# Performance work log

Hardware: AMD Instinct MI355X
Metric: run time of the kernel (lower is better)

## Reference

```python
import jax, jax.numpy as jnp
import numpy as np

N, E, IN, H, C, T = 50000, 800000, 128, 64, 64, 2
F1, FO1 = H, H // T   # conv1: per-tower in/out feats
F2, FO2 = H, C // T   # conv2
STD_EPS = 1e-5
BN_EPS = 1e-5


def setup_inputs() -> dict:
    key = jax.random.key(0)
    ks = jax.random.split(key, 12)
    rn = lambda k, s, sc=0.05: jax.random.normal(k, s, jnp.float32) * sc
    return {
        "x": jax.random.normal(ks[0], (N, IN), jnp.float32),
        "embed_W": rn(ks[1], (IN, H)),
        "embed_b": jnp.zeros((H,), jnp.float32),
        "pre_W1": rn(ks[2], (T, 2 * F1, F1)),
        "pre_b1": jnp.zeros((T, F1), jnp.float32),
        "post_W1": rn(ks[3], (T, 13 * F1, FO1)),
        "post_b1": jnp.zeros((T, FO1), jnp.float32),
        "lin_W1": rn(ks[4], (H, H)),
        "lin_b1": jnp.zeros((H,), jnp.float32),
        "bn_gamma": jnp.ones((H,), jnp.float32),
        "bn_beta": jnp.zeros((H,), jnp.float32),
        "pre_W2": rn(ks[5], (T, 2 * F2, F2)),
        "pre_b2": jnp.zeros((T, F2), jnp.float32),
        "post_W2": rn(ks[6], (T, 13 * F2, FO2)),
        "post_b2": jnp.zeros((T, FO2), jnp.float32),
        "lin_W2": rn(ks[7], (C, C)),
        "lin_b2": jnp.zeros((C,), jnp.float32),
        "src": jax.random.randint(ks[8], (E,), 0, N, jnp.int32),
        "dst": jax.random.randint(ks[9], (E,), 0, N, jnp.int32),
    }


def _pna_conv(h, src, dst, deg_raw, degc, avg_log, preW, preb, postW, postb, linW, linb):
    # h: [N, F] node feats; messages flow src -> dst, aggregated at dst.
    m = jnp.concatenate([h[dst], h[src]], axis=-1)            # [E, 2F]  (cat[x_i, x_j])
    m = jnp.einsum('ef,tfg->etg', m, preW) + preb[None]       # [E, T, F] per-tower pre-NN
    seg = lambda v: jax.ops.segment_sum(v, dst, num_segments=N)
    cnt = degc[:, None, None]                                 # clamped degree >= 1
    has = (deg_raw > 0)[:, None, None]
    mean = seg(m) / cnt                                       # [N, T, F]
    mean_sq = seg(m * m) / cnt
    mn = jnp.where(has, jax.ops.segment_min(m, dst, num_segments=N), 0.0)
    mx = jnp.where(has, jax.ops.segment_max(m, dst, num_segments=N), 0.0)
    std = jnp.sqrt(jax.nn.relu(mean_sq - mean * mean) + STD_EPS)
    agg = jnp.concatenate([mean, mn, mx, std], axis=-1)       # [N, T, 4F]
    ld = jnp.log(degc + 1.0)[:, None, None]
    out = jnp.concatenate([agg, agg * (ld / avg_log), agg * (avg_log / ld)], axis=-1)  # [N, T, 12F]
    F = h.shape[-1]
    out = jnp.concatenate([jnp.broadcast_to(h[:, None, :], (N, T, F)), out], axis=-1)  # [N, T, 13F]
    out = jnp.einsum('ntf,tfg->ntg', out, postW) + postb[None]  # [N, T, FO] per-tower post-NN
    return out.reshape(N, -1) @ linW + linb                    # final mixing Linear(out, out)


def reference(x, embed_W, embed_b, pre_W1, pre_b1, post_W1, post_b1, lin_W1, lin_b1,
              bn_gamma, bn_beta, pre_W2, pre_b2, post_W2, post_b2, lin_W2, lin_b2,
              src, dst):
    deg_raw = jax.ops.segment_sum(jnp.ones((E,), jnp.float32), dst, num_segments=N)
    degc = jnp.maximum(deg_raw, 1.0)
    avg_log = jnp.mean(jnp.log(deg_raw + 1.0))  # avg_deg['log'] from the graph's degrees
    h = x @ embed_W + embed_b
    h = _pna_conv(h, src, dst, deg_raw, degc, avg_log,
                  pre_W1, pre_b1, post_W1, post_b1, lin_W1, lin_b1)
    mu = jnp.mean(h, axis=0)
    var = jnp.mean((h - mu) ** 2, axis=0)
    h = bn_gamma * (h - mu) / jnp.sqrt(var + BN_EPS) + bn_beta
    h = jax.nn.relu(h)  # dropout is identity in eval mode
    return _pna_conv(h, src, dst, deg_raw, degc, avg_log,
                     pre_W2, pre_b2, post_W2, post_b2, lin_W2, lin_b2)
```

## Files before the change

kernel.cpp:

```cpp
#include <hip/hip_runtime.h>

#define N_NODES 50000
#define E_EDGES 800000
#define IN_F    128
#define H_F     64
#define STD_EPS 1e-5f
#define BN_EPS  1e-5f

__global__ __launch_bounds__(256) void k_hist(const int* __restrict__ dst,
                                              int* __restrict__ deg) {
  int e = blockIdx.x * 256 + threadIdx.x;
  if (e < E_EDGES) atomicAdd(&deg[dst[e]], 1);
}

__global__ __launch_bounds__(256) void k_scan_part(const int* __restrict__ deg,
                                                   int* __restrict__ partials,
                                                   float* __restrict__ scalars) {
  __shared__ int red[256];
  __shared__ float redf[256];
  int base = blockIdx.x * 1024;
  int s = 0; float ls = 0.f;
  for (int j = threadIdx.x; j < 1024; j += 256) {
    int i = base + j;
    if (i < N_NODES) { int d = deg[i]; s += d; ls += logf((float)d + 1.0f); }
  }
  red[threadIdx.x] = s; redf[threadIdx.x] = ls; __syncthreads();
  for (int st = 128; st > 0; st >>= 1) {
    if (threadIdx.x < st) {
      red[threadIdx.x] += red[threadIdx.x + st];
      redf[threadIdx.x] += redf[threadIdx.x + st];
    }
    __syncthreads();
  }
  if (threadIdx.x == 0) {
    partials[blockIdx.x] = red[0];
    atomicAdd(&scalars[0], redf[0]);
  }
}

__global__ void k_scan_mid(int* __restrict__ partials, int nblk,
                           float* __restrict__ scalars) {
  if (threadIdx.x == 0) {
    int run = 0;
    for (int b = 0; b < nblk; b++) { int v = partials[b]; partials[b] = run; run += v; }
    scalars[1] = scalars[0] / (float)N_NODES;
  }
}

__global__ __launch_bounds__(256) void k_scan_final(const int* __restrict__ deg,
                                                    const int* __restrict__ partials,
                                                    int* __restrict__ row_ptr,
                                                    int* __restrict__ cursor) {
  __shared__ int ts[256];
  int base = blockIdx.x * 1024 + threadIdx.x * 4;
  int d[4]; int s = 0;
#pragma unroll
  for (int j = 0; j < 4; j++) {
    int i = base + j;
    d[j] = (i < N_NODES) ? deg[i] : 0;
    s += d[j];
  }
  ts[threadIdx.x] = s; __syncthreads();
  for (int off = 1; off < 256; off <<= 1) {
    int t = (threadIdx.x >= off) ? ts[threadIdx.x - off] : 0;
    __syncthreads();
    ts[threadIdx.x] += t;
    __syncthreads();
  }
  int excl = (threadIdx.x > 0) ? ts[threadIdx.x - 1] : 0;
  int run = partials[blockIdx.x] + excl;
#pragma unroll
  for (int j = 0; j < 4; j++) {
    int i = base + j;
    if (i < N_NODES) { row_ptr[i] = run; cursor[i] = run; run += d[j]; }
  }
  if (blockIdx.x == 0 && threadIdx.x == 0) row_ptr[N_NODES] = E_EDGES;
}

__global__ __launch_bounds__(256) void k_scatter(const int* __restrict__ src,
                                                 const int* __restrict__ dst,
                                                 int* __restrict__ cursor,
                                                 int* __restrict__ csr_src) {
  int e = blockIdx.x * 256 + threadIdx.x;
  if (e < E_EDGES) {
    int d = dst[e];
    int p = atomicAdd(&cursor[d], 1);
    csr_src[p] = src[e];
  }
}

__global__ __launch_bounds__(256) void k_transpose(const float* __restrict__ pW1,
                                                   const float* __restrict__ pW2,
                                                   const float* __restrict__ lW1,
                                                   const float* __restrict__ lW2,
                                                   float* __restrict__ pWT,
                                                   float* __restrict__ lWT) {
  int idx = blockIdx.x * 256 + threadIdx.x;
  if (idx < 106496) {
    int layer = idx / 53248, r = idx % 53248;
    int t = r / 26624, r2 = r % 26624;
    int fb = r2 / 128, r3 = r2 % 128;
    int g = r3 / 4, j = r3 % 4;
    const float* srcp = layer ? pW2 : pW1;
    pWT[idx] = srcp[(size_t)t * 26624 + (fb * 4 + j) * 32 + g];
  } else if (idx < 114688) {
    int jj = idx - 106496;
    int layer = jj / 4096, r2 = jj % 4096;
    int c4 = r2 / 256, r3 = r2 % 256;
    int col = r3 / 4, j = r3 % 4;
    const float* srcl = layer ? lW2 : lW1;
    lWT[jj] = srcl[(c4 * 4 + j) * 64 + col];
  }
}

__global__ __launch_bounds__(256) void k_embed(const float* __restrict__ x,
                                               const float* __restrict__ W,
                                               const float* __restrict__ bias,
                                               float* __restrict__ h) {
  __shared__ float sW[IN_F * 64];
  __shared__ float sx[IN_F * 36];
  for (int i = threadIdx.x; i < IN_F * 64; i += 256) sW[i] = W[i];
  int f = threadIdx.x & 63, ng = threadIdx.x >> 6;
  float bj = bias[f];
  const int NGRP = (N_NODES + 31) / 32;
  for (int grp = blockIdx.x; grp < NGRP; grp += gridDim.x) {
    int n0 = grp * 32;
    __syncthreads();
    for (int idx = threadIdx.x; idx < 32 * IN_F; idx += 256) {
      int nl = idx >> 7, k = idx & 127;
      int n = n0 + nl;
      sx[k * 36 + nl] = (n < N_NODES) ? x[(size_t)n * IN_F + k] : 0.f;
    }
    __syncthreads();
    float a[8] = {bj, bj, bj, bj, bj, bj, bj, bj};
    const float* xp = &sx[ng * 8];
#pragma unroll 4
    for (int k = 0; k < IN_F; k++) {
      float4 h0 = *(const float4*)&xp[k * 36];
      float4 h1 = *(const float4*)&xp[k * 36 + 4];
      float w = sW[k * 64 + f];
      a[0] = fmaf(h0.x, w, a[0]); a[1] = fmaf(h0.y, w, a[1]);
      a[2] = fmaf(h0.z, w, a[2]); a[3] = fmaf(h0.w, w, a[3]);
      a[4] = fmaf(h1.x, w, a[4]); a[5] = fmaf(h1.y, w, a[5]);
      a[6] = fmaf(h1.z, w, a[6]); a[7] = fmaf(h1.w, w, a[7]);
    }
#pragma unroll
    for (int j = 0; j < 8; j++) {
      int n = n0 + ng * 8 + j;
      if (n < N_NODES) h[(size_t)n * 64 + f] = a[j];
    }
  }
}

template <bool BN>
__global__ __launch_bounds__(256) void k_preab(const float* __restrict__ hin,
                                               const float* __restrict__ preW,
                                               const float* __restrict__ preb,
                                               const float* __restrict__ bnscale,
                                               const float* __restrict__ bnshift,
                                               float* __restrict__ h2out,
                                               float* __restrict__ hA,
                                               float* __restrict__ hB) {
  __shared__ float sWp[64 * 128];
  __shared__ float sh[64 * 36];
  int t = blockIdx.x & 1;
  const float* Wsrc = preW + (size_t)t * 128 * 64;
  for (int i = threadIdx.x; i < 64 * 64; i += 256) {
    int k = i >> 6, f = i & 63;
    float wa = Wsrc[k * 64 + f];
    float wb = Wsrc[(64 + k) * 64 + f];
    *(float2*)&sWp[k * 128 + f * 2] = make_float2(wa, wb);
  }
  int f = threadIdx.x & 63, ng = threadIdx.x >> 6;
  float pb = preb[t * 64 + f];
  int nblk2 = gridDim.x >> 1;
  const int NGRP = (N_NODES + 31) / 32;
  for (int grp = blockIdx.x >> 1; grp < NGRP; grp += nblk2) {
    int n0 = grp * 32;
    __syncthreads();
    for (int idx = threadIdx.x; idx < 32 * 64; idx += 256) {
      int nl = idx >> 6, k = idx & 63;
      int n = n0 + nl;
      float v = 0.f;
      if (n < N_NODES) {
        v = hin[(size_t)n * 64 + k];
        if (BN) {
          v = fmaxf(fmaf(v, bnscale[k], bnshift[k]), 0.f);
          if (t == 0) h2out[(size_t)n * 64 + k] = v;
        }
      }
      sh[k * 36 + nl] = v;
    }
    __syncthreads();
    float a[8] = {pb, pb, pb, pb, pb, pb, pb, pb};
    float b[8] = {0, 0, 0, 0, 0, 0, 0, 0};
    const float* hp = &sh[ng * 8];
    const float* wp = &sWp[f * 2];
#pragma unroll 4
    for (int k = 0; k < 64; k++) {
      float4 h0 = *(const float4*)&hp[k * 36];
      float4 h1 = *(const float4*)&hp[k * 36 + 4];
      float2 w2 = *(const float2*)&wp[k * 128];
      a[0] = fmaf(h0.x, w2.x, a[0]); b[0] = fmaf(h0.x, w2.y, b[0]);
      a[1] = fmaf(h0.y, w2.x, a[1]); b[1] = fmaf(h0.y, w2.y, b[1]);
      a[2] = fmaf(h0.z, w2.x, a[2]); b[2] = fmaf(h0.z, w2.y, b[2]);
      a[3] = fmaf(h0.w, w2.x, a[3]); b[3] = fmaf(h0.w, w2.y, b[3]);
      a[4] = fmaf(h1.x, w2.x, a[4]); b[4] = fmaf(h1.x, w2.y, b[4]);
      a[5] = fmaf(h1.y, w2.x, a[5]); b[5] = fmaf(h1.y, w2.y, b[5]);
      a[6] = fmaf(h1.z, w2.x, a[6]); b[6] = fmaf(h1.z, w2.y, b[6]);
      a[7] = fmaf(h1.w, w2.x, a[7]); b[7] = fmaf(h1.w, w2.y, b[7]);
    }
    int tf = t * 64 + f;
#pragma unroll
    for (int j = 0; j < 8; j++) {
      int n = n0 + ng * 8 + j;
      if (n < N_NODES) {
        hA[(size_t)n * 128 + tf] = a[j];
        hB[(size_t)n * 128 + tf] = b[j];
      }
    }
  }
}

__global__ __launch_bounds__(256, 7) void k_conv(const float* __restrict__ hA,
                                                 const float* __restrict__ hB,
                                                 const float* __restrict__ hskip,
                                                 const int* __restrict__ row_ptr,
                                                 const int* __restrict__ csr_src,
                                                 const float* __restrict__ postWT,
                                                 const float* __restrict__ postb,
                                                 const float* __restrict__ linWT,
                                                 const float* __restrict__ linb,
                                                 const float* __restrict__ scalars,
                                                 float* __restrict__ out) {
  __shared__ float sm[2 * 5 * 8 * 64];
  __shared__ float sAB[16];
  int w = threadIdx.x >> 6, lane = threadIdx.x & 63;
  int n0 = blockIdx.x * 8;
  int t = lane >> 5, fb2 = (lane & 31) * 2;
  int off = t * 64 + fb2;
  float avg = scalars[1];

#pragma unroll 1
  for (int k = 0; k < 2; k++) {
    int nl = w * 2 + k;
    int n = n0 + nl;
    float2 a = *(const float2*)&hA[(size_t)n * 128 + off];
    int rp0 = __builtin_amdgcn_readfirstlane(row_ptr[n]);
    int rp1 = __builtin_amdgcn_readfirstlane(row_ptr[n + 1]);
    float sx0=0,sy0=0,qx0=0,qy0=0, sx1=0,sy1=0,qx1=0,qy1=0;
    float mnx0=INFINITY,mny0=INFINITY,mxx0=-INFINITY,mxy0=-INFINITY;
    float mnx1=INFINITY,mny1=INFINITY,mxx1=-INFINITY,mxy1=-INFINITY;
    int i = rp0;
    int end4 = rp0 + ((rp1 - rp0) & ~3);
    if (i < end4) {
      int s0 = csr_src[i], s1 = csr_src[i+1], s2 = csr_src[i+2], s3 = csr_src[i+3];
      while (true) {
        float2 v0 = *(const float2*)&hB[(size_t)s0 * 128 + off];
        float2 v1 = *(const float2*)&hB[(size_t)s1 * 128 + off];
        float2 v2 = *(const float2*)&hB[(size_t)s2 * 128 + off];
        float2 v3 = *(const float2*)&hB[(size_t)s3 * 128 + off];
        i += 4;
        bool more = (i < end4);
        if (more) { s0 = csr_src[i]; s1 = csr_src[i+1]; s2 = csr_src[i+2]; s3 = csr_src[i+3]; }
        float e0x = v0.x + a.x, e0y = v0.y + a.y;
        float e1x = v1.x + a.x, e1y = v1.y + a.y;
        float e2x = v2.x + a.x, e2y = v2.y + a.y;
        float e3x = v3.x + a.x, e3y = v3.y + a.y;
        sx0 += e0x; qx0 = fmaf(e0x,e0x,qx0); mnx0 = fminf(mnx0,e0x); mxx0 = fmaxf(mxx0,e0x);
        sy0 += e0y; qy0 = fmaf(e0y,e0y,qy0); mny0 = fminf(mny0,e0y); mxy0 = fmaxf(mxy0,e0y);
        sx1 += e1x; qx1 = fmaf(e1x,e1x,qx1); mnx1 = fminf(mnx1,e1x); mxx1 = fmaxf(mxx1,e1x);
        sy1 += e1y; qy1 = fmaf(e1y,e1y,qy1); mny1 = fminf(mny1,e1y); mxy1 = fmaxf(mxy1,e1y);
        sx0 += e2x; qx0 = fmaf(e2x,e2x,qx0); mnx0 = fminf(mnx0,e2x); mxx0 = fmaxf(mxx0,e2x);
        sy0 += e2y; qy0 = fmaf(e2y,e2y,qy0); mny0 = fminf(mny0,e2y); mxy0 = fmaxf(mxy0,e2y);
        sx1 += e3x; qx1 = fmaf(e3x,e3x,qx1); mnx1 = fminf(mnx1,e3x); mxx1 = fmaxf(mxx1,e3x);
        sy1 += e3y; qy1 = fmaf(e3y,e3y,qy1); mny1 = fminf(mny1,e3y); mxy1 = fmaxf(mxy1,e3y);
        if (!more) break;
      }
    }
    {
      int r = rp1 - i;
      if (r > 0) {
        int e1i = (r > 1) ? i + 1 : i;
        int e2i = (r > 2) ? i + 2 : i;
        int t0 = csr_src[i], t1 = csr_src[e1i], t2 = csr_src[e2i];
        float2 u0 = *(const float2*)&hB[(size_t)t0 * 128 + off];
        float2 u1 = *(const float2*)&hB[(size_t)t1 * 128 + off];
        float2 u2 = *(const float2*)&hB[(size_t)t2 * 128 + off];
        float ex = u0.x + a.x, ey = u0.y + a.y;
        sx0 += ex; qx0 = fmaf(ex,ex,qx0); mnx0 = fminf(mnx0,ex); mxx0 = fmaxf(mxx0,ex);
        sy0 += ey; qy0 = fmaf(ey,ey,qy0); mny0 = fminf(mny0,ey); mxy0 = fmaxf(mxy0,ey);
        if (r > 1) {
          ex = u1.x + a.x; ey = u1.y + a.y;
          sx1 += ex; qx1 = fmaf(ex,ex,qx1); mnx1 = fminf(mnx1,ex); mxx1 = fmaxf(mxx1,ex);
          sy1 += ey; qy1 = fmaf(ey,ey,qy1); mny1 = fminf(mny1,ey); mxy1 = fmaxf(mxy1,ey);
        }
        if (r > 2) {
          ex = u2.x + a.x; ey = u2.y + a.y;
          sx0 += ex; qx0 = fmaf(ex,ex,qx0); mnx0 = fminf(mnx0,ex); mxx0 = fmaxf(mxx0,ex);
          sy0 += ey; qy0 = fmaf(ey,ey,qy0); mny0 = fminf(mny0,ey); mxy0 = fmaxf(mxy0,ey);
        }
      }
    }
    int dg = rp1 - rp0;
    float cnt = (float)(dg > 0 ? dg : 1);
    float inv = 1.0f / cnt;
    float meanx = (sx0 + sx1) * inv, meany = (sy0 + sy1) * inv;
    float qx = qx0 + qx1, qy = qy0 + qy1;
    float sdx = sqrtf(fmaxf(qx * inv - meanx * meanx, 0.f) + STD_EPS);
    float sdy = sqrtf(fmaxf(qy * inv - meany * meany, 0.f) + STD_EPS);
    float mnx = fminf(mnx0, mnx1), mny = fminf(mny0, mny1);
    float mxx = fmaxf(mxx0, mxx1), mxy = fmaxf(mxy0, mxy1);
    if (dg == 0) { mnx = 0; mny = 0; mxx = 0; mxy = 0; }
    float ldv = logf(cnt + 1.f);
    float2 hsv = *(const float2*)&hskip[(size_t)n * 64 + fb2];
    float* bp = &sm[t * 2560 + nl * 64 + fb2];
    *(float2*)&bp[0]    = hsv;
    *(float2*)&bp[512]  = make_float2(meanx, meany);
    *(float2*)&bp[1024] = make_float2(mnx, mny);
    *(float2*)&bp[1536] = make_float2(mxx, mxy);
    *(float2*)&bp[2048] = make_float2(sdx, sdy);
    if (lane == 0) { sAB[nl] = ldv / avg; sAB[8 + nl] = avg / ldv; }
  }
  __syncthreads();

  float g1[8] = {0,0,0,0,0,0,0,0};
  float g2[8] = {0,0,0,0,0,0,0,0};
  float g3[8] = {0,0,0,0,0,0,0,0};
  {
    int g = lane & 31, hf0 = w * 16, fb0 = w * 4;
    const float4* pw4 = (const float4*)postWT + (size_t)t * 6656 + g;
    const float* vb = &sm[t * 2560 + hf0];
#pragma unroll
    for (int jj = 0; jj < 4; jj++) {
      float4 wv = pw4[(fb0 + jj) * 32];
#pragma unroll
      for (int nn = 0; nn < 8; nn++) {
        float4 v = *(const float4*)&vb[nn * 64 + jj * 4];
        g1[nn] = fmaf(v.w, wv.w, fmaf(v.z, wv.z, fmaf(v.y, wv.y, fmaf(v.x, wv.x, g1[nn]))));
      }
    }
#pragma unroll
    for (int fa = 0; fa < 4; fa++) {
      const float* vfa = &vb[(1 + fa) * 512];
#pragma unroll
      for (int jj = 0; jj < 4; jj++) {
        int fb = 16 + fa * 16 + fb0 + jj;
        float4 w1v = pw4[fb * 32];
        float4 w2v = pw4[(fb + 64) * 32];
        float4 w3v = pw4[(fb + 128) * 32];
#pragma unroll
        for (int nn = 0; nn < 8; nn++) {
          float4 v = *(const float4*)&vfa[nn * 64 + jj * 4];
          g1[nn] = fmaf(v.w, w1v.w, fmaf(v.z, w1v.z, fmaf(v.y, w1v.y, fmaf(v.x, w1v.x, g1[nn]))));
          g2[nn] = fmaf(v.w, w2v.w, fmaf(v.z, w2v.z, fmaf(v.y, w2v.y, fmaf(v.x, w2v.x, g2[nn]))));
          g3[nn] = fmaf(v.w, w3v.w, fmaf(v.z, w3v.z, fmaf(v.y, w3v.y, fmaf(v.x, w3v.x, g3[nn]))));
        }
      }
    }
  }
  float o8[8];
#pragma unroll
  for (int nn = 0; nn < 8; nn++)
    o8[nn] = fmaf(sAB[8 + nn], g3[nn], fmaf(sAB[nn], g2[nn], g1[nn]));
  __syncthreads();

  {
    int sw = (w + (lane >> 4)) & 3;
#pragma unroll
    for (int nn = 0; nn < 8; nn++)
      sm[((nn * 64 + lane) << 2) + sw] = o8[nn];
  }
  __syncthreads();

  {
#pragma unroll
    for (int r = 0; r < 2; r++) {
      int idx = r * 256 + (int)threadIdx.x;
      float4 p = *(const float4*)&sm[idx << 2];
      sm[2048 + idx] = p.x + p.y + p.z + p.w + postb[idx & 63];
    }
  }
  __syncthreads();

  {
    float acc0 = linb[lane], acc1 = acc0;
    const float4* lw4 = (const float4*)linWT + lane;
    const float* p0 = &sm[2048 + (w * 2) * 64];
    const float* p1 = p0 + 64;
#pragma unroll
    for (int c4 = 0; c4 < 16; c4++) {
      float4 lwv = lw4[c4 * 64];
      float4 pa = *(const float4*)&p0[c4 * 4];
      float4 pb2 = *(const float4*)&p1[c4 * 4];
      acc0 = fmaf(pa.w, lwv.w, fmaf(pa.z, lwv.z, fmaf(pa.y, lwv.y, fmaf(pa.x, lwv.x, acc0))));
      acc1 = fmaf(pb2.w, lwv.w, fmaf(pb2.z, lwv.z, fmaf(pb2.y, lwv.y, fmaf(pb2.x, lwv.x, acc1))));
    }
    size_t ob = (size_t)(n0 + w * 2) * 64 + lane;
    out[ob] = acc0;
    out[ob + 64] = acc1;
  }
}

__global__ __launch_bounds__(256) void k_bnstats(const float* __restrict__ y,
                                                 float* __restrict__ bnsum,
                                                 float* __restrict__ bnsumsq) {
  __shared__ float r1[256], r2[256];
  int c = threadIdx.x & 63, r = threadIdx.x >> 6;
  float s = 0, q = 0;
  for (int n = blockIdx.x * 4 + r; n < N_NODES; n += gridDim.x * 4) {
    float v = y[(size_t)n * 64 + c];
    s += v; q = fmaf(v, v, q);
  }
  r1[threadIdx.x] = s; r2[threadIdx.x] = q; __syncthreads();
  if (threadIdx.x < 64) {
    s = r1[threadIdx.x] + r1[threadIdx.x + 64] + r1[threadIdx.x + 128] + r1[threadIdx.x + 192];
    q = r2[threadIdx.x] + r2[threadIdx.x + 64] + r2[threadIdx.x + 128] + r2[threadIdx.x + 192];
    atomicAdd(&bnsum[threadIdx.x], s);
    atomicAdd(&bnsumsq[threadIdx.x], q);
  }
}

__global__ void k_bnfin(const float* __restrict__ bnsum, const float* __restrict__ bnsumsq,
                        const float* __restrict__ gamma, const float* __restrict__ beta,
                        float* __restrict__ bnscale, float* __restrict__ bnshift) {
  int c = threadIdx.x;
  if (c < 64) {
    float mu = bnsum[c] * (1.f / N_NODES);
    float var = bnsumsq[c] * (1.f / N_NODES) - mu * mu;
    float sc = gamma[c] / sqrtf(var + BN_EPS);
    bnscale[c] = sc;
    bnshift[c] = fmaf(-mu, sc, beta[c]);
  }
}

extern "C" void kernel_launch(void* const* d_in, const int* in_sizes, int n_in,
                              void* d_out, int out_size, void* d_ws, size_t ws_size,
                              hipStream_t stream) {
  const float* x      = (const float*)d_in[0];
  const float* embW   = (const float*)d_in[1];
  const float* embB   = (const float*)d_in[2];
  const float* preW1  = (const float*)d_in[3];
  const float* preb1  = (const float*)d_in[4];
  const float* postW1 = (const float*)d_in[5];
  const float* postb1 = (const float*)d_in[6];
  const float* linW1  = (const float*)d_in[7];
  const float* linb1  = (const float*)d_in[8];
  const float* gamma  = (const float*)d_in[9];
  const float* beta   = (const float*)d_in[10];
  const float* preW2  = (const float*)d_in[11];
  const float* preb2  = (const float*)d_in[12];
  const float* postW2 = (const float*)d_in[13];
  const float* postb2 = (const float*)d_in[14];
  const float* linW2  = (const float*)d_in[15];
  const float* linb2  = (const float*)d_in[16];
  const int*   src    = (const int*)d_in[17];
  const int*   dst    = (const int*)d_in[18];
  float* out = (float*)d_out;

  char* w = (char*)d_ws;
  size_t o = 0;
  int*   deg     = (int*)(w + o);   o += (size_t)N_NODES * 4;
  float* scalars = (float*)(w + o); o += 64;
  float* bnsum   = (float*)(w + o); o += 256;
  float* bnsumsq = (float*)(w + o); o += 256;
  float* bnscale = (float*)(w + o); o += 256;
  float* bnshift = (float*)(w + o); o += 256;
  size_t zero_len = o;
  o = (o + 255) & ~(size_t)255;
  int* partials = (int*)(w + o);  o += 256;
  int* row_ptr  = (int*)(w + o);  o += (size_t)(N_NODES + 1) * 4; o = (o + 255) & ~(size_t)255;
  int* cursor   = (int*)(w + o);  o += (size_t)N_NODES * 4;       o = (o + 255) & ~(size_t)255;
  int* csr      = (int*)(w + o);  o += (size_t)E_EDGES * 4;       o = (o + 255) & ~(size_t)255;
  float* postWT = (float*)(w + o); o += (size_t)2 * 53248 * 4;
  float* linWT  = (float*)(w + o); o += (size_t)2 * 4096 * 4;
  float* h1 = (float*)(w + o); o += (size_t)N_NODES * 64 * 4;
  float* y1 = (float*)(w + o); o += (size_t)N_NODES * 64 * 4;
  float* h2 = (float*)(w + o); o += (size_t)N_NODES * 64 * 4;
  float* hA = (float*)(w + o); o += (size_t)N_NODES * 128 * 4;
  float* hB = (float*)(w + o); o += (size_t)N_NODES * 128 * 4;

  hipMemsetAsync(w, 0, zero_len, stream);

  const int NBLK_SCAN = (N_NODES + 1023) / 1024;
  k_hist<<<(E_EDGES + 255) / 256, 256, 0, stream>>>(dst, deg);
  k_scan_part<<<NBLK_SCAN, 256, 0, stream>>>(deg, partials, scalars);
  k_scan_mid<<<1, 64, 0, stream>>>(partials, NBLK_SCAN, scalars);
  k_scan_final<<<NBLK_SCAN, 256, 0, stream>>>(deg, partials, row_ptr, cursor);
  k_scatter<<<(E_EDGES + 255) / 256, 256, 0, stream>>>(src, dst, cursor, csr);
  k_transpose<<<448, 256, 0, stream>>>(postW1, postW2, linW1, linW2, postWT, linWT);

  k_embed<<<768, 256, 0, stream>>>(x, embW, embB, h1);

  k_preab<false><<<768, 256, 0, stream>>>(h1, preW1, preb1, nullptr, nullptr, nullptr, hA, hB);
  k_conv<<<N_NODES / 8, 256, 0, stream>>>(hA, hB, h1, row_ptr, csr,
                                          postWT, postb1, linWT, linb1, scalars, y1);
  k_bnstats<<<256, 256, 0, stream>>>(y1, bnsum, bnsumsq);
  k_bnfin<<<1, 64, 0, stream>>>(bnsum, bnsumsq, gamma, beta, bnscale, bnshift);

  k_preab<true><<<768, 256, 0, stream>>>(y1, preW2, preb2, bnscale, bnshift, h2, hA, hB);
  k_conv<<<N_NODES / 8, 256, 0, stream>>>(hA, hB, h2, row_ptr, csr,
                                          postWT + 53248, postb2, linWT + 4096, linb2,
                                          scalars, out);
}
```

Before: 544.0 us.

## Merge setup kernels, fold BN stats into conv, widen preab tile

Several small setup kernels are merged into combined launches: the degree histogram with the embedding, and the scan partials with the weight transpose. The single-thread scan-mid kernel is removed, with each scan-final block summing the partials before it. BatchNorm statistics are accumulated by atomics inside the first conv, and the BN finalize is folded into the preab kernel, which removes the bnstats pass over y1 and two launches. Preab now processes 64 nodes per tile with 16 accumulators per thread. This adds atomic contention on 64 addresses and more register pressure in exchange for fewer launches and one less read of y1.

```diff
diff --git a/kernel.cpp b/kernel.cpp
--- a/kernel.cpp
+++ b/kernel.cpp
@@ -7,95 +7,90 @@
 #define STD_EPS 1e-5f
 #define BN_EPS  1e-5f
 
-__global__ __launch_bounds__(256) void k_hist(const int* __restrict__ dst,
-                                              int* __restrict__ deg) {
-  int e = blockIdx.x * 256 + threadIdx.x;
-  if (e < E_EDGES) atomicAdd(&deg[dst[e]], 1);
-}
-
-__global__ __launch_bounds__(256) void k_scan_part(const int* __restrict__ deg,
-                                                   int* __restrict__ partials,
-                                                   float* __restrict__ scalars) {
+#define HIST_BLK 3125
+#define EMB_BLK  768
+#define SCAN_BLK 49
+#define TRANS_BLK 448
+
+__global__ __launch_bounds__(256) void k_hist_embed(const int* __restrict__ dst,
+                                                    int* __restrict__ deg,
+                                                    const float* __restrict__ x,
+                                                    const float* __restrict__ W,
+                                                    const float* __restrict__ bias,
+                                                    float* __restrict__ h) {
+  __shared__ float sW[IN_F * 64];
+  __shared__ float sx[IN_F * 36];
+  if (blockIdx.x < HIST_BLK) {
+    int e = blockIdx.x * 256 + threadIdx.x;
+    atomicAdd(&deg[dst[e]], 1);
+    return;
+  }
+  for (int i = threadIdx.x; i < IN_F * 64; i += 256) sW[i] = W[i];
+  int f = threadIdx.x & 63, ng = threadIdx.x >> 6;
+  float bj = bias[f];
+  const int NGRP = (N_NODES + 31) / 32;
+  for (int grp = blockIdx.x - HIST_BLK; grp < NGRP; grp += EMB_BLK) {
+    int n0 = grp * 32;
+    __syncthreads();
+    for (int idx = threadIdx.x; idx < 32 * IN_F; idx += 256) {
+      int nl = idx >> 7, k = idx & 127;
+      int n = n0 + nl;
+      sx[k * 36 + nl] = (n < N_NODES) ? x[(size_t)n * IN_F + k] : 0.f;
+    }
+    __syncthreads();
+    float a[8] = {bj, bj, bj, bj, bj, bj, bj, bj};
+    const float* xp = &sx[ng * 8];
+#pragma unroll 4
+    for (int k = 0; k < IN_F; k++) {
+      float4 h0 = *(const float4*)&xp[k * 36];
+      float4 h1 = *(const float4*)&xp[k * 36 + 4];
+      float w = sW[k * 64 + f];
+      a[0] = fmaf(h0.x, w, a[0]); a[1] = fmaf(h0.y, w, a[1]);
+      a[2] = fmaf(h0.z, w, a[2]); a[3] = fmaf(h0.w, w, a[3]);
+      a[4] = fmaf(h1.x, w, a[4]); a[5] = fmaf(h1.y, w, a[5]);
+      a[6] = fmaf(h1.z, w, a[6]); a[7] = fmaf(h1.w, w, a[7]);
+    }
+#pragma unroll
+    for (int j = 0; j < 8; j++) {
+      int n = n0 + ng * 8 + j;
+      if (n < N_NODES) h[(size_t)n * 64 + f] = a[j];
+    }
+  }
+}
+
+__global__ __launch_bounds__(256) void k_scanpart_trans(const int* __restrict__ deg,
+                                                        int* __restrict__ partials,
+                                                        float* __restrict__ scalars,
+                                                        const float* __restrict__ pW1,
+                                                        const float* __restrict__ pW2,
+                                                        const float* __restrict__ lW1,
+                                                        const float* __restrict__ lW2,
+                                                        float* __restrict__ pWT,
+                                                        float* __restrict__ lWT) {
   __shared__ int red[256];
   __shared__ float redf[256];
-  int base = blockIdx.x * 1024;
-  int s = 0; float ls = 0.f;
-  for (int j = threadIdx.x; j < 1024; j += 256) {
-    int i = base + j;
-    if (i < N_NODES) { int d = deg[i]; s += d; ls += logf((float)d + 1.0f); }
-  }
-  red[threadIdx.x] = s; redf[threadIdx.x] = ls; __syncthreads();
-  for (int st = 128; st > 0; st >>= 1) {
-    if (threadIdx.x < st) {
-      red[threadIdx.x] += red[threadIdx.x + st];
-      redf[threadIdx.x] += redf[threadIdx.x + st];
-    }
-    __syncthreads();
-  }
-  if (threadIdx.x == 0) {
-    partials[blockIdx.x] = red[0];
-    atomicAdd(&scalars[0], redf[0]);
-  }
-}
-
-__global__ void k_scan_mid(int* __restrict__ partials, int nblk,
-                           float* __restrict__ scalars) {
-  if (threadIdx.x == 0) {
-    int run = 0;
-    for (int b = 0; b < nblk; b++) { int v = partials[b]; partials[b] = run; run += v; }
-    scalars[1] = scalars[0] / (float)N_NODES;
-  }
-}
-
-__global__ __launch_bounds__(256) void k_scan_final(const int* __restrict__ deg,
-                                                    const int* __restrict__ partials,
-                                                    int* __restrict__ row_ptr,
-                                                    int* __restrict__ cursor) {
-  __shared__ int ts[256];
-  int base = blockIdx.x * 1024 + threadIdx.x * 4;
-  int d[4]; int s = 0;
-#pragma unroll
-  for (int j = 0; j < 4; j++) {
-    int i = base + j;
-    d[j] = (i < N_NODES) ? deg[i] : 0;
-    s += d[j];
-  }
-  ts[threadIdx.x] = s; __syncthreads();
-  for (int off = 1; off < 256; off <<= 1) {
-    int t = (threadIdx.x >= off) ? ts[threadIdx.x - off] : 0;
-    __syncthreads();
-    ts[threadIdx.x] += t;
-    __syncthreads();
-  }
-  int excl = (threadIdx.x > 0) ? ts[threadIdx.x - 1] : 0;
-  int run = partials[blockIdx.x] + excl;
-#pragma unroll
-  for (int j = 0; j < 4; j++) {
-    int i = base + j;
-    if (i < N_NODES) { row_ptr[i] = run; cursor[i] = run; run += d[j]; }
-  }
-  if (blockIdx.x == 0 && threadIdx.x == 0) row_ptr[N_NODES] = E_EDGES;
-}
-
-__global__ __launch_bounds__(256) void k_scatter(const int* __restrict__ src,
-                                                 const int* __restrict__ dst,
-                                                 int* __restrict__ cursor,
-                                                 int* __restrict__ csr_src) {
-  int e = blockIdx.x * 256 + threadIdx.x;
-  if (e < E_EDGES) {
-    int d = dst[e];
-    int p = atomicAdd(&cursor[d], 1);
-    csr_src[p] = src[e];
-  }
-}
-
-__global__ __launch_bounds__(256) void k_transpose(const float* __restrict__ pW1,
-                                                   const float* __restrict__ pW2,
-                                                   const float* __restrict__ lW1,
-                                                   const float* __restrict__ lW2,
-                                                   float* __restrict__ pWT,
-                                                   float* __restrict__ lWT) {
-  int idx = blockIdx.x * 256 + threadIdx.x;
+  if (blockIdx.x < SCAN_BLK) {
+    int base = blockIdx.x * 1024;
+    int s = 0; float ls = 0.f;
+    for (int j = threadIdx.x; j < 1024; j += 256) {
+      int i = base + j;
+      if (i < N_NODES) { int d = deg[i]; s += d; ls += logf((float)d + 1.0f); }
+    }
+    red[threadIdx.x] = s; redf[threadIdx.x] = ls; __syncthreads();
+    for (int st = 128; st > 0; st >>= 1) {
+      if (threadIdx.x < st) {
+        red[threadIdx.x] += red[threadIdx.x + st];
+        redf[threadIdx.x] += redf[threadIdx.x + st];
+      }
+      __syncthreads();
+    }
+    if (threadIdx.x == 0) {
+      partials[blockIdx.x] = red[0];
+      atomicAdd(&scalars[0], redf[0]);
+    }
+    return;
+  }
+  int idx = (blockIdx.x - SCAN_BLK) * 256 + threadIdx.x;
   if (idx < 106496) {
     int layer = idx / 53248, r = idx % 53248;
     int t = r / 26624, r2 = r % 26624;
@@ -113,42 +108,55 @@
   }
 }
 
-__global__ __launch_bounds__(256) void k_embed(const float* __restrict__ x,
-                                               const float* __restrict__ W,
-                                               const float* __restrict__ bias,
-                                               float* __restrict__ h) {
-  __shared__ float sW[IN_F * 64];
-  __shared__ float sx[IN_F * 36];
-  for (int i = threadIdx.x; i < IN_F * 64; i += 256) sW[i] = W[i];
-  int f = threadIdx.x & 63, ng = threadIdx.x >> 6;
-  float bj = bias[f];
-  const int NGRP = (N_NODES + 31) / 32;
-  for (int grp = blockIdx.x; grp < NGRP; grp += gridDim.x) {
-    int n0 = grp * 32;
+__global__ __launch_bounds__(256) void k_scan_final(const int* __restrict__ deg,
+                                                    const int* __restrict__ partials,
+                                                    int* __restrict__ row_ptr,
+                                                    int* __restrict__ cursor,
+                                                    float* __restrict__ scalars) {
+  __shared__ int ts[256];
+  __shared__ int sbase;
+  if (threadIdx.x == 0) {
+    int pre = 0;
+    for (int b = 0; b < (int)blockIdx.x; b++) pre += partials[b];
+    sbase = pre;
+    if (blockIdx.x == 0) {
+      scalars[1] = scalars[0] / (float)N_NODES;
+      row_ptr[N_NODES] = E_EDGES;
+    }
+  }
+  int base = blockIdx.x * 1024 + threadIdx.x * 4;
+  int d[4]; int s = 0;
+#pragma unroll
+  for (int j = 0; j < 4; j++) {
+    int i = base + j;
+    d[j] = (i < N_NODES) ? deg[i] : 0;
+    s += d[j];
+  }
+  ts[threadIdx.x] = s; __syncthreads();
+  for (int off = 1; off < 256; off <<= 1) {
+    int t = (threadIdx.x >= off) ? ts[threadIdx.x - off] : 0;
     __syncthreads();
-    for (int idx = threadIdx.x; idx < 32 * IN_F; idx += 256) {
-      int nl = idx >> 7, k = idx & 127;
-      int n = n0 + nl;
-      sx[k * 36 + nl] = (n < N_NODES) ? x[(size_t)n * IN_F + k] : 0.f;
-    }
+    ts[threadIdx.x] += t;
     __syncthreads();
-    float a[8] = {bj, bj, bj, bj, bj, bj, bj, bj};
-    const float* xp = &sx[ng * 8];
-#pragma unroll 4
-    for (int k = 0; k < IN_F; k++) {
-      float4 h0 = *(const float4*)&xp[k * 36];
-      float4 h1 = *(const float4*)&xp[k * 36 + 4];
-      float w = sW[k * 64 + f];
-      a[0] = fmaf(h0.x, w, a[0]); a[1] = fmaf(h0.y, w, a[1]);
-      a[2] = fmaf(h0.z, w, a[2]); a[3] = fmaf(h0.w, w, a[3]);
-      a[4] = fmaf(h1.x, w, a[4]); a[5] = fmaf(h1.y, w, a[5]);
-      a[6] = fmaf(h1.z, w, a[6]); a[7] = fmaf(h1.w, w, a[7]);
-    }
-#pragma unroll
-    for (int j = 0; j < 8; j++) {
-      int n = n0 + ng * 8 + j;
-      if (n < N_NODES) h[(size_t)n * 64 + f] = a[j];
-    }
+  }
+  int excl = (threadIdx.x > 0) ? ts[threadIdx.x - 1] : 0;
+  int run = sbase + excl;
+#pragma unroll
+  for (int j = 0; j < 4; j++) {
+    int i = base + j;
+    if (i < N_NODES) { row_ptr[i] = run; cursor[i] = run; run += d[j]; }
+  }
+}
+
+__global__ __launch_bounds__(256) void k_scatter(const int* __restrict__ src,
+                                                 const int* __restrict__ dst,
+                                                 int* __restrict__ cursor,
+                                                 int* __restrict__ csr_src) {
+  int e = blockIdx.x * 256 + threadIdx.x;
+  if (e < E_EDGES) {
+    int d = dst[e];
+    int p = atomicAdd(&cursor[d], 1);
+    csr_src[p] = src[e];
   }
 }
 
@@ -156,13 +164,16 @@
 __global__ __launch_bounds__(256) void k_preab(const float* __restrict__ hin,
                                                const float* __restrict__ preW,
                                                const float* __restrict__ preb,
-                                               const float* __restrict__ bnscale,
-                                               const float* __restrict__ bnshift,
+                                               const float* __restrict__ bnsum,
+                                               const float* __restrict__ bnsumsq,
+                                               const float* __restrict__ gamma,
+                                               const float* __restrict__ beta,
                                                float* __restrict__ h2out,
                                                float* __restrict__ hA,
                                                float* __restrict__ hB) {
   __shared__ float sWp[64 * 128];
-  __shared__ float sh[64 * 36];
+  __shared__ float sh[64 * 68];
+  __shared__ float sbn[128];
   int t = blockIdx.x & 1;
   const float* Wsrc = preW + (size_t)t * 128 * 64;
   for (int i = threadIdx.x; i < 64 * 64; i += 256) {
@@ -171,49 +182,68 @@
     float wb = Wsrc[(64 + k) * 64 + f];
     *(float2*)&sWp[k * 128 + f * 2] = make_float2(wa, wb);
   }
+  if (BN && threadIdx.x < 64) {
+    int c = threadIdx.x;
+    float mu = bnsum[c] * (1.f / N_NODES);
+    float var = bnsumsq[c] * (1.f / N_NODES) - mu * mu;
+    float sc = gamma[c] / sqrtf(var + BN_EPS);
+    sbn[c] = sc;
+    sbn[64 + c] = fmaf(-mu, sc, beta[c]);
+  }
   int f = threadIdx.x & 63, ng = threadIdx.x >> 6;
   float pb = preb[t * 64 + f];
   int nblk2 = gridDim.x >> 1;
-  const int NGRP = (N_NODES + 31) / 32;
+  const int NGRP = (N_NODES + 63) / 64;
   for (int grp = blockIdx.x >> 1; grp < NGRP; grp += nblk2) {
-    int n0 = grp * 32;
+    int n0 = grp * 64;
     __syncthreads();
-    for (int idx = threadIdx.x; idx < 32 * 64; idx += 256) {
+    for (int idx = threadIdx.x; idx < 64 * 64; idx += 256) {
       int nl = idx >> 6, k = idx & 63;
       int n = n0 + nl;
       float v = 0.f;
       if (n < N_NODES) {
         v = hin[(size_t)n * 64 + k];
         if (BN) {
-          v = fmaxf(fmaf(v, bnscale[k], bnshift[k]), 0.f);
+          v = fmaxf(fmaf(v, sbn[k], sbn[64 + k]), 0.f);
           if (t == 0) h2out[(size_t)n * 64 + k] = v;
         }
       }
-      sh[k * 36 + nl] = v;
+      sh[k * 68 + nl] = v;
     }
     __syncthreads();
-    float a[8] = {pb, pb, pb, pb, pb, pb, pb, pb};
-    float b[8] = {0, 0, 0, 0, 0, 0, 0, 0};
-    const float* hp = &sh[ng * 8];
+    float a[16], b[16];
+#pragma unroll
+    for (int j = 0; j < 16; j++) { a[j] = pb; b[j] = 0.f; }
+    const float* hp = &sh[ng * 16];
     const float* wp = &sWp[f * 2];
-#pragma unroll 4
+#pragma unroll 2
     for (int k = 0; k < 64; k++) {
-      float4 h0 = *(const float4*)&hp[k * 36];
-      float4 h1 = *(const float4*)&hp[k * 36 + 4];
+      float4 h0 = *(const float4*)&hp[k * 68];
+      float4 h1 = *(const float4*)&hp[k * 68 + 4];
+      float4 h2 = *(const float4*)&hp[k * 68 + 8];
+      float4 h3 = *(const float4*)&hp[k * 68 + 12];
       float2 w2 = *(const float2*)&wp[k * 128];
-      a[0] = fmaf(h0.x, w2.x, a[0]); b[0] = fmaf(h0.x, w2.y, b[0]);
-      a[1] = fmaf(h0.y, w2.x, a[1]); b[1] = fmaf(h0.y, w2.y, b[1]);
-      a[2] = fmaf(h0.z, w2.x, a[2]); b[2] = fmaf(h0.z, w2.y, b[2]);
-      a[3] = fmaf(h0.w, w2.x, a[3]); b[3] = fmaf(h0.w, w2.y, b[3]);
-      a[4] = fmaf(h1.x, w2.x, a[4]); b[4] = fmaf(h1.x, w2.y, b[4]);
-      a[5] = fmaf(h1.y, w2.x, a[5]); b[5] = fmaf(h1.y, w2.y, b[5]);
-      a[6] = fmaf(h1.z, w2.x, a[6]); b[6] = fmaf(h1.z, w2.y, b[6]);
-      a[7] = fmaf(h1.w, w2.x, a[7]); b[7] = fmaf(h1.w, w2.y, b[7]);
+      a[0]  = fmaf(h0.x, w2.x, a[0]);  b[0]  = fmaf(h0.x, w2.y, b[0]);
+      a[1]  = fmaf(h0.y, w2.x, a[1]);  b[1]  = fmaf(h0.y, w2.y, b[1]);
+      a[2]  = fmaf(h0.z, w2.x, a[2]);  b[2]  = fmaf(h0.z, w2.y, b[2]);
+      a[3]  = fmaf(h0.w, w2.x, a[3]);  b[3]  = fmaf(h0.w, w2.y, b[3]);
+      a[4]  = fmaf(h1.x, w2.x, a[4]);  b[4]  = fmaf(h1.x, w2.y, b[4]);
+      a[5]  = fmaf(h1.y, w2.x, a[5]);  b[5]  = fmaf(h1.y, w2.y, b[5]);
+      a[6]  = fmaf(h1.z, w2.x, a[6]);  b[6]  = fmaf(h1.z, w2.y, b[6]);
+      a[7]  = fmaf(h1.w, w2.x, a[7]);  b[7]  = fmaf(h1.w, w2.y, b[7]);
+      a[8]  = fmaf(h2.x, w2.x, a[8]);  b[8]  = fmaf(h2.x, w2.y, b[8]);
+      a[9]  = fmaf(h2.y, w2.x, a[9]);  b[9]  = fmaf(h2.y, w2.y, b[9]);
+      a[10] = fmaf(h2.z, w2.x, a[10]); b[10] = fmaf(h2.z, w2.y, b[10]);
+      a[11] = fmaf(h2.w, w2.x, a[11]); b[11] = fmaf(h2.w, w2.y, b[11]);
+      a[12] = fmaf(h3.x, w2.x, a[12]); b[12] = fmaf(h3.x, w2.y, b[12]);
+      a[13] = fmaf(h3.y, w2.x, a[13]); b[13] = fmaf(h3.y, w2.y, b[13]);
+      a[14] = fmaf(h3.z, w2.x, a[14]); b[14] = fmaf(h3.z, w2.y, b[14]);
+      a[15] = fmaf(h3.w, w2.x, a[15]); b[15] = fmaf(h3.w, w2.y, b[15]);
     }
     int tf = t * 64 + f;
 #pragma unroll
-    for (int j = 0; j < 8; j++) {
-      int n = n0 + ng * 8 + j;
+    for (int j = 0; j < 16; j++) {
+      int n = n0 + ng * 16 + j;
       if (n < N_NODES) {
         hA[(size_t)n * 128 + tf] = a[j];
         hB[(size_t)n * 128 + tf] = b[j];
@@ -222,6 +252,7 @@
   }
 }
 
+template <bool BNACC>
 __global__ __launch_bounds__(256, 7) void k_conv(const float* __restrict__ hA,
                                                  const float* __restrict__ hB,
                                                  const float* __restrict__ hskip,
@@ -232,7 +263,9 @@
                                                  const float* __restrict__ linWT,
                                                  const float* __restrict__ linb,
                                                  const float* __restrict__ scalars,
-                                                 float* __restrict__ out) {
+                                                 float* __restrict__ out,
+                                                 float* __restrict__ bnsum,
+                                                 float* __restrict__ bnsumsq) {
   __shared__ float sm[2 * 5 * 8 * 64];
   __shared__ float sAB[16];
   int w = threadIdx.x >> 6, lane = threadIdx.x & 63;
@@ -399,38 +432,10 @@
     size_t ob = (size_t)(n0 + w * 2) * 64 + lane;
     out[ob] = acc0;
     out[ob + 64] = acc1;
-  }
-}
-
-__global__ __launch_bounds__(256) void k_bnstats(const float* __restrict__ y,
-                                                 float* __restrict__ bnsum,
-                                                 float* __restrict__ bnsumsq) {
-  __shared__ float r1[256], r2[256];
-  int c = threadIdx.x & 63, r = threadIdx.x >> 6;
-  float s = 0, q = 0;
-  for (int n = blockIdx.x * 4 + r; n < N_NODES; n += gridDim.x * 4) {
-    float v = y[(size_t)n * 64 + c];
-    s += v; q = fmaf(v, v, q);
-  }
-  r1[threadIdx.x] = s; r2[threadIdx.x] = q; __syncthreads();
-  if (threadIdx.x < 64) {
-    s = r1[threadIdx.x] + r1[threadIdx.x + 64] + r1[threadIdx.x + 128] + r1[threadIdx.x + 192];
-    q = r2[threadIdx.x] + r2[threadIdx.x + 64] + r2[threadIdx.x + 128] + r2[threadIdx.x + 192];
-    atomicAdd(&bnsum[threadIdx.x], s);
-    atomicAdd(&bnsumsq[threadIdx.x], q);
-  }
-}
-
-__global__ void k_bnfin(const float* __restrict__ bnsum, const float* __restrict__ bnsumsq,
-                        const float* __restrict__ gamma, const float* __restrict__ beta,
-                        float* __restrict__ bnscale, float* __restrict__ bnshift) {
-  int c = threadIdx.x;
-  if (c < 64) {
-    float mu = bnsum[c] * (1.f / N_NODES);
-    float var = bnsumsq[c] * (1.f / N_NODES) - mu * mu;
-    float sc = gamma[c] / sqrtf(var + BN_EPS);
-    bnscale[c] = sc;
-    bnshift[c] = fmaf(-mu, sc, beta[c]);
+    if (BNACC) {
+      atomicAdd(&bnsum[lane], acc0 + acc1);
+      atomicAdd(&bnsumsq[lane], fmaf(acc0, acc0, acc1 * acc1));
+    }
   }
 }
 
@@ -464,8 +469,6 @@
   float* scalars = (float*)(w + o); o += 64;
   float* bnsum   = (float*)(w + o); o += 256;
   float* bnsumsq = (float*)(w + o); o += 256;
-  float* bnscale = (float*)(w + o); o += 256;
-  float* bnshift = (float*)(w + o); o += 256;
   size_t zero_len = o;
   o = (o + 255) & ~(size_t)255;
   int* partials = (int*)(w + o);  o += 256;
@@ -482,24 +485,20 @@
 
   hipMemsetAsync(w, 0, zero_len, stream);
 
-  const int NBLK_SCAN = (N_NODES + 1023) / 1024;
-  k_hist<<<(E_EDGES + 255) / 256, 256, 0, stream>>>(dst, deg);
-  k_scan_part<<<NBLK_SCAN, 256, 0, stream>>>(deg, partials, scalars);
-  k_scan_mid<<<1, 64, 0, stream>>>(partials, NBLK_SCAN, scalars);
-  k_scan_final<<<NBLK_SCAN, 256, 0, stream>>>(deg, partials, row_ptr, cursor);
+  k_hist_embed<<<HIST_BLK + EMB_BLK, 256, 0, stream>>>(dst, deg, x, embW, embB, h1);
+  k_scanpart_trans<<<SCAN_BLK + TRANS_BLK, 256, 0, stream>>>(
+      deg, partials, scalars, postW1, postW2, linW1, linW2, postWT, linWT);
+  k_scan_final<<<SCAN_BLK, 256, 0, stream>>>(deg, partials, row_ptr, cursor, scalars);
   k_scatter<<<(E_EDGES + 255) / 256, 256, 0, stream>>>(src, dst, cursor, csr);
-  k_transpose<<<448, 256, 0, stream>>>(postW1, postW2, linW1, linW2, postWT, linWT);
-
-  k_embed<<<768, 256, 0, stream>>>(x, embW, embB, h1);
-
-  k_preab<false><<<768, 256, 0, stream>>>(h1, preW1, preb1, nullptr, nullptr, nullptr, hA, hB);
-  k_conv<<<N_NODES / 8, 256, 0, stream>>>(hA, hB, h1, row_ptr, csr,
-                                          postWT, postb1, linWT, linb1, scalars, y1);
-  k_bnstats<<<256, 256, 0, stream>>>(y1, bnsum, bnsumsq);
-  k_bnfin<<<1, 64, 0, stream>>>(bnsum, bnsumsq, gamma, beta, bnscale, bnshift);
-
-  k_preab<true><<<768, 256, 0, stream>>>(y1, preW2, preb2, bnscale, bnshift, h2, hA, hB);
-  k_conv<<<N_NODES / 8, 256, 0, stream>>>(hA, hB, h2, row_ptr, csr,
-                                          postWT + 53248, postb2, linWT + 4096, linb2,
-                                          scalars, out);
-}
+
+  k_preab<false><<<768, 256, 0, stream>>>(h1, preW1, preb1, nullptr, nullptr,
+                                          nullptr, nullptr, nullptr, hA, hB);
+  k_conv<true><<<N_NODES / 8, 256, 0, stream>>>(hA, hB, h1, row_ptr, csr,
+                                                postWT, postb1, linWT, linb1,
+                                                scalars, y1, bnsum, bnsumsq);
+  k_preab<true><<<768, 256, 0, stream>>>(y1, preW2, preb2, bnsum, bnsumsq,
+                                         gamma, beta, h2, hA, hB);
+  k_conv<false><<<N_NODES / 8, 256, 0, stream>>>(hA, hB, h2, row_ptr, csr,
+                                                 postWT + 53248, postb2, linWT + 4096,
+                                                 linb2, scalars, out, nullptr, nullptr);
+}
```

After: 1.038 ms. +90.8%, slower.
